# Optimization experiments

Measured on AMD Instinct MI355X. Metric: run time of the kernel, lower is better.

The kernel has to match this reference:

```python
import jax, jax.numpy as jnp
import numpy as np

C = 1024
H = 64
W = 64


def _conv1x1(x, Wt, b):
    # x: [1, Cin, H, W], Wt: [Cout, Cin] -> [1, Cout, H, W]
    return jnp.einsum('oc,bchw->bohw', Wt, x) + b[None, :, None, None]


def setup_inputs() -> dict:
    key = jax.random.key(0)
    ks = jax.random.split(key, 12)
    sc = 1.0 / np.sqrt(C)
    return {
        'x_f': jax.random.normal(ks[0], (1, C, H, W), jnp.float32),
        'x_m': jax.random.normal(ks[1], (1, C, H, W), jnp.float32),
        'x_l': jax.random.normal(ks[2], (1, C, H, W), jnp.float32),
        'Wq': jax.random.normal(ks[3], (C // 2, C), jnp.float32) * sc,
        'bq': jax.random.normal(ks[4], (C // 2,), jnp.float32) * sc,
        'Wk1': jax.random.normal(ks[5], (C // 2, C), jnp.float32) * sc,
        'bk1': jax.random.normal(ks[6], (C // 2,), jnp.float32) * sc,
        'Wk2': jax.random.normal(ks[7], (C // 2, C), jnp.float32) * sc,
        'bk2': jax.random.normal(ks[8], (C // 2,), jnp.float32) * sc,
        'Wv': jax.random.normal(ks[9], (C, C), jnp.float32) * sc,
        'bv': jax.random.normal(ks[10], (C,), jnp.float32) * sc,
        'gamma': jax.random.normal(ks[11], (1,), jnp.float32),
    }


def reference(x_f, x_m, x_l, Wq, bq, Wk1, bk1, Wk2, bk2, Wv, bv, gamma):
    c = x_f.shape[1]
    h, w = x_f.shape[2], x_f.shape[3]
    # torch .view(1, C, -1) on a [1, C/2, H, W] tensor: row-major reshape to [C, H*W/2]
    q = _conv1x1(x_m, Wq, bq).reshape(c, -1).T      # [HW/2, C]
    kf = _conv1x1(x_f, Wk1, bk1).reshape(c, -1)     # [C, HW/2]
    kl = _conv1x1(x_l, Wk2, bk2).reshape(c, -1)     # [C, HW/2]
    att_f = jax.nn.softmax(kf @ q, axis=-1)         # [C, C]
    att_l = jax.nn.softmax(kl @ q, axis=-1)         # [C, C]
    v = _conv1x1(x_m, Wv, bv).reshape(c, -1)        # [C, HW]
    out = att_f @ v + att_l @ v                     # [C, HW]
    out = out.reshape(1, c, h, w)
    return gamma * out + (x_l + x_f) / 2
```

## Files before the change

kernel.cpp:

```cpp
#include <hip/hip_runtime.h>
#include <math.h>


typedef __attribute__((ext_vector_type(8))) short    bf16x8;
typedef __attribute__((ext_vector_type(4))) float    f32x4;

__device__ __forceinline__ unsigned short f2bf(float x) {
    unsigned u = __float_as_uint(x);
    u += 0x7FFFu + ((u >> 16) & 1u);
    return (unsigned short)(u >> 16);
}
__device__ __forceinline__ float bf2f(unsigned short h) {
    return __uint_as_float(((unsigned)h) << 16);
}
__device__ __forceinline__ void split2(float x, unsigned short& h, unsigned short& l) {
    h = f2bf(x);
    l = f2bf(x - bf2f(h));
}

__device__ __forceinline__ size_t swz(int m, int k, int kpan) {
    return ((size_t)((m >> 4) * kpan + (k >> 5))) * 512
         + (size_t)((((k >> 3) & 3) * 16 + (m & 15)) * 8 + (k & 7));
}

__device__ __forceinline__ void gld16(const unsigned short* g, unsigned short* l) {
    __builtin_amdgcn_global_load_lds(
        (const __attribute__((address_space(1))) unsigned int*)g,
        (__attribute__((address_space(3))) unsigned int*)l,
        16, 0, 0);
}

__device__ __forceinline__ bf16x8 gload16(const unsigned short* p) {
    bf16x8 r;
    asm volatile("global_load_dwordx4 %0, %1, off"
                 : "=v"(r) : "v"(p) : "memory");
    return r;
}

#define RAW_BARRIER() asm volatile("s_barrier" ::: "memory")

template<int N>
__device__ __forceinline__ void vmwait() {
    asm volatile("s_waitcnt vmcnt(%0)" :: "i"(N) : "memory");
}

__global__ __launch_bounds__(256) void weights_split_k(
    const float* __restrict__ Wq, const float* __restrict__ Wk1,
    const float* __restrict__ Wk2, const float* __restrict__ Wv,
    unsigned short* __restrict__ Wqh, unsigned short* __restrict__ Wql,
    unsigned short* __restrict__ Wk1h, unsigned short* __restrict__ Wk1l,
    unsigned short* __restrict__ Wk2h, unsigned short* __restrict__ Wk2l,
    unsigned short* __restrict__ Wvh, unsigned short* __restrict__ Wvl)
{
    const int gi = blockIdx.x;
    const float* src; unsigned short *H, *L; int base;
    if (gi < 512)       { src = Wq;  H = Wqh;  L = Wql;  base = gi; }
    else if (gi < 1024) { src = Wk1; H = Wk1h; L = Wk1l; base = gi - 512; }
    else if (gi < 1536) { src = Wk2; H = Wk2h; L = Wk2l; base = gi - 1024; }
    else                { src = Wv;  H = Wvh;  L = Wvl;  base = gi - 1536; }
    const size_t i = (size_t)base * 1024 + threadIdx.x * 4;
    const int m = (int)(i >> 10);
    const int k = (int)(i & 1023);
    const float4 v = *(const float4*)(src + i);
    ushort4 h, l;
    split2(v.x, h.x, l.x); split2(v.y, h.y, l.y);
    split2(v.z, h.z, l.z); split2(v.w, h.w, l.w);
    const size_t o = swz(m, k, 32);
    *(ushort4*)(H + o) = h;
    *(ushort4*)(L + o) = l;
}

__global__ __launch_bounds__(256) void transpose3_k(
    const float* __restrict__ x0, const float* __restrict__ x1,
    const float* __restrict__ x2,
    unsigned short* __restrict__ t0h, unsigned short* __restrict__ t0l,
    unsigned short* __restrict__ t1h, unsigned short* __restrict__ t1l,
    unsigned short* __restrict__ t2h, unsigned short* __restrict__ t2l)
{
    const float* X; unsigned short *Th, *Tl;
    if (blockIdx.z == 0)      { X = x0; Th = t0h; Tl = t0l; }
    else if (blockIdx.z == 1) { X = x1; Th = t1h; Tl = t1l; }
    else                      { X = x2; Th = t2h; Tl = t2l; }

    __shared__ float t[32 * 33];
    const int tid = threadIdx.x;
    const int c0 = blockIdx.y * 32;
    const int p0 = blockIdx.x * 32;

    const int cl = tid >> 3;
    const int p4 = (tid & 7) * 4;
    const float4 v = *(const float4*)(X + (size_t)(c0 + cl) * 4096 + p0 + p4);
    t[(p4 + 0) * 33 + cl] = v.x;
    t[(p4 + 1) * 33 + cl] = v.y;
    t[(p4 + 2) * 33 + cl] = v.z;
    t[(p4 + 3) * 33 + cl] = v.w;
    __syncthreads();

    const int pl = tid >> 3;
    const int c4 = (tid & 7) * 4;
    ushort4 h, l;
    split2(t[pl * 33 + c4 + 0], h.x, l.x);
    split2(t[pl * 33 + c4 + 1], h.y, l.y);
    split2(t[pl * 33 + c4 + 2], h.z, l.z);
    split2(t[pl * 33 + c4 + 3], h.w, l.w);
    const size_t o = (size_t)(p0 + pl) * 1024 + c0 + c4;
    *(ushort4*)(Th + o) = h;
    *(ushort4*)(Tl + o) = l;
}

__global__ __launch_bounds__(256) void transpose1_k(
    const float* __restrict__ X,
    unsigned short* __restrict__ Th, unsigned short* __restrict__ Tl)
{
    __shared__ float t[32 * 33];
    const int tid = threadIdx.x;
    const int c0 = blockIdx.y * 32;
    const int p0 = blockIdx.x * 32;

    const int cl = tid >> 3;
    const int p4 = (tid & 7) * 4;
    const float4 v = *(const float4*)(X + (size_t)(c0 + cl) * 4096 + p0 + p4);
    t[(p4 + 0) * 33 + cl] = v.x;
    t[(p4 + 1) * 33 + cl] = v.y;
    t[(p4 + 2) * 33 + cl] = v.z;
    t[(p4 + 3) * 33 + cl] = v.w;
    __syncthreads();

    const int pl = tid >> 3;
    const int c4 = (tid & 7) * 4;
    ushort4 h, l;
    split2(t[pl * 33 + c4 + 0], h.x, l.x);
    split2(t[pl * 33 + c4 + 1], h.y, l.y);
    split2(t[pl * 33 + c4 + 2], h.z, l.z);
    split2(t[pl * 33 + c4 + 3], h.w, l.w);
    const size_t o = (size_t)(p0 + pl) * 1024 + c0 + c4;
    *(ushort4*)(Th + o) = h;
    *(ushort4*)(Tl + o) = l;
}

template<int TERMS, int NJ>
__device__ __forceinline__ void gemm_core(
    const unsigned short* __restrict__ Ah, const unsigned short* __restrict__ Al,
    const unsigned short* __restrict__ Bh, const unsigned short* __restrict__ Bl,
    int ldkB, int kpanA, int kbeg, int kend, int m0, int n0,
    unsigned short* Bs_h, unsigned short* Bs_l,
    f32x4 (&acc)[4][NJ])
{
    const int tid  = threadIdx.x;
    const int lane = tid & 63;
    const int wv   = tid >> 6;
    const int wm   = (wv >> 1) * 64;
    const int wn   = (wv & 1) * (16 * NJ);
    const int lr   = lane & 15;
    const int quad = lane >> 4;
    const int BUFE = 1024 * NJ;
    constexpr int AOPS = (TERMS == 3 ? 8 : 4);
    constexpr int VM_FULL = AOPS + NJ + NJ;
    constexpr int VM_MID  = AOPS + NJ;

    const unsigned short* gsrc = (wv < 2) ? Bh : Bl;
    unsigned short* ldst = (wv < 2) ? Bs_h : Bs_l;
    const int tt0  = (wv & 1) * NJ;
    const int lrow = lane >> 2;
    const int gseg = ((lane & 3) - ((lane >> 3) & 3)) & 3;
    const size_t bstep = (size_t)16 * (size_t)ldkB;
    const unsigned short* gp0 =
        gsrc + (size_t)(n0 + tt0 * 16 + lrow) * ldkB + kbeg + gseg * 8;

    const int pk0 = kbeg >> 5;
    const size_t astr  = (size_t)kpanA * 512;
    const size_t abase = (size_t)((m0 + wm) >> 4) * astr + (size_t)pk0 * 512
                       + (size_t)lane * 8;
    const unsigned short* ap0 = Ah + abase;
    const unsigned short* al0 = (TERMS == 3) ? (Al + abase) : nullptr;

    const int rdseg = (quad + (lr >> 1)) & 3;

    const int nsteps = (kend - kbeg) >> 5;

#pragma unroll
    for (int u = 0; u < NJ; ++u)
        gld16(gp0 + (size_t)u * bstep, ldst + 0 * BUFE + (tt0 + u) * 512);

    bf16x8 cah[4], cal[4], nah[4], nal[4];
#pragma unroll
    for (int i = 0; i < 4; ++i) {
        cah[i] = gload16(ap0 + (size_t)i * astr);
        if (TERMS == 3) cal[i] = gload16(al0 + (size_t)i * astr);
    }
#pragma unroll
    for (int u = 0; u < NJ; ++u)
        gld16(gp0 + (size_t)u * bstep + 32, ldst + 1 * BUFE + (tt0 + u) * 512);

    int br = 0;
    int bw = 2;

#define GSTEP(S, CH, CL, NH, NL)                                              \
    {                                                                         \
        RAW_BARRIER();                                                        \
        const bool hasA = (S) + 1 < nsteps;                                   \
        const bool hasD = (S) + 2 < nsteps;                                   \
        if (hasA) {                                                           \
            const size_t aoff = (size_t)((S) + 1) * 512;                      \
            _Pragma("unroll")                                                 \
            for (int i = 0; i < 4; ++i) {                                     \
                NH[i] = gload16(ap0 + (size_t)i * astr + aoff);               \
                if (TERMS == 3)                                               \
                    NL[i] = gload16(al0 + (size_t)i * astr + aoff);           \
            }                                                                 \
        }                                                                     \
        if (hasD) {                                                           \
            const size_t goff = (size_t)((S) + 2) * 32;                       \
            unsigned short* dst = ldst + bw * BUFE;                           \
            _Pragma("unroll")                                                 \
            for (int u = 0; u < NJ; ++u)                                      \
                gld16(gp0 + (size_t)u * bstep + goff, dst + (tt0 + u) * 512); \
            vmwait<VM_FULL>();                                                \
        } else if (hasA) {                                                    \
            vmwait<VM_MID>();                                                 \
        } else {                                                              \
            vmwait<0>();                                                      \
        }                                                                     \
        RAW_BARRIER();                                                        \
        __builtin_amdgcn_sched_barrier(0);                                    \
        const int rbase = br * BUFE + (wn + lr) * 32 + rdseg * 8;             \
        _Pragma("unroll")                                                     \
        for (int j = 0; j < NJ; ++j) {                                        \
            const bf16x8 bh = *(const bf16x8*)(Bs_h + rbase + j * 512);       \
            const bf16x8 bl = *(const bf16x8*)(Bs_l + rbase + j * 512);       \
            _Pragma("unroll")                                                 \
            for (int i = 0; i < 4; ++i) {                                     \
                acc[i][j] = __builtin_amdgcn_mfma_f32_16x16x32_bf16(          \
                    CH[i], bh, acc[i][j], 0, 0, 0);                           \
                acc[i][j] = __builtin_amdgcn_mfma_f32_16x16x32_bf16(          \
                    CH[i], bl, acc[i][j], 0, 0, 0);                           \
                if (TERMS == 3)                                               \
                    acc[i][j] = __builtin_amdgcn_mfma_f32_16x16x32_bf16(      \
                        CL[i], bh, acc[i][j], 0, 0, 0);                       \
            }                                                                 \
        }                                                                     \
        br = (br == 2) ? 0 : br + 1;                                          \
        bw = (bw == 2) ? 0 : bw + 1;                                          \
    }

    for (int s = 0; s < nsteps; s += 2) {
        GSTEP(s,     cah, cal, nah, nal);
        GSTEP(s + 1, nah, nal, cah, cal);
    }
#undef GSTEP
}

#define GEMM_PROLOGUE(NJ_)                                              \
    __shared__ __align__(16) unsigned short Bs_h[3 * 1024 * (NJ_)];     \
    __shared__ __align__(16) unsigned short Bs_l[3 * 1024 * (NJ_)];     \
    f32x4 acc[4][(NJ_)];                                                \
    _Pragma("unroll") for (int i = 0; i < 4; ++i)                       \
    _Pragma("unroll") for (int j = 0; j < (NJ_); ++j)                   \
    _Pragma("unroll") for (int r = 0; r < 4; ++r) acc[i][j][r] = 0.f;   \
    const int lane = threadIdx.x & 63;                                  \
    const int wv   = threadIdx.x >> 6;                                  \
    const int wm   = (wv >> 1) * 64;                                    \
    const int wn   = (wv & 1) * (16 * (NJ_));                           \
    const int lr   = lane & 15;                                         \
    const int quad = lane >> 4;                                         \
    (void)lane; (void)wv; (void)wm; (void)wn;

__global__ __launch_bounds__(256, 2) void conv_all_k(
    const unsigned short* __restrict__ Wqh, const unsigned short* __restrict__ Wql,
    const unsigned short* __restrict__ Wk1h, const unsigned short* __restrict__ Wk1l,
    const unsigned short* __restrict__ Wk2h, const unsigned short* __restrict__ Wk2l,
    const unsigned short* __restrict__ Wvh, const unsigned short* __restrict__ Wvl,
    const unsigned short* __restrict__ xmTh, const unsigned short* __restrict__ xmTl,
    const unsigned short* __restrict__ xfTh, const unsigned short* __restrict__ xfTl,
    const unsigned short* __restrict__ xlTh, const unsigned short* __restrict__ xlTl,
    const float* __restrict__ bq, const float* __restrict__ bk1,
    const float* __restrict__ bk2, const float* __restrict__ bv,
    unsigned short* __restrict__ Qh, unsigned short* __restrict__ Ql,
    unsigned short* __restrict__ Kfh, unsigned short* __restrict__ Kfl,
    unsigned short* __restrict__ Klh, unsigned short* __restrict__ Kll,
    float* __restrict__ V)
{
    GEMM_PROLOGUE(4);
    const int lid = blockIdx.y * 32 + blockIdx.x;
    const int wg  = (lid & 7) * 80 + (lid >> 3);
    const int mt  = wg >> 5;
    const int n0  = (wg & 31) * 128;

    const unsigned short *Ah, *Al, *Bh, *Bl;
    const float* bias;
    unsigned short *Ch = nullptr, *Cl = nullptr;
    float* Cv = nullptr;
    int mloc, mode;
    if (mt < 4) {
        Ah = Wqh;  Al = Wql;  Bh = xmTh; Bl = xmTl; bias = bq;
        Ch = Qh;   Cl = Ql;   mloc = mt * 128;        mode = 0;
    } else if (mt < 8) {
        Ah = Wk1h; Al = Wk1l; Bh = xfTh; Bl = xfTl; bias = bk1;
        Ch = Kfh;  Cl = Kfl;  mloc = (mt - 4) * 128;  mode = 1;
    } else if (mt < 12) {
        Ah = Wk2h; Al = Wk2l; Bh = xlTh; Bl = xlTl; bias = bk2;
        Ch = Klh;  Cl = Kll;  mloc = (mt - 8) * 128;  mode = 1;
    } else {
        Ah = Wvh;  Al = Wvl;  Bh = xmTh; Bl = xmTl; bias = bv;
        Cv = V;    mloc = (mt - 12) * 128;            mode = 2;
    }

    gemm_core<3, 4>(Ah, Al, Bh, Bl, 1024, 32, 0, 1024, mloc, n0, Bs_h, Bs_l, acc);

#pragma unroll
    for (int i = 0; i < 4; ++i) {
        const int mb = mloc + wm + i * 16 + quad * 4;
#pragma unroll
        for (int j = 0; j < 4; ++j) {
            const int nn = n0 + wn + j * 16 + lr;
#pragma unroll
            for (int r = 0; r < 4; ++r) {
                const float v = acc[i][j][r] + bias[mb + r];
                if (mode == 2) {
                    Cv[(size_t)(mb + r) * 4096 + nn] = v;
                } else if (mode == 0) {
                    unsigned short h, l;
                    split2(v, h, l);
                    const size_t idx = (size_t)(mb + r) * 4096 + nn;
                    Ch[idx] = h;
                    Cl[idx] = l;
                } else {
                    const int m2 = ((mb + r) << 1) | (nn >> 11);
                    const int k2 = nn & 2047;
                    const size_t o = swz(m2, k2, 64);
                    unsigned short h, l;
                    split2(v, h, l);
                    Ch[o] = h;
                    Cl[o] = l;
                }
            }
        }
    }
}

__global__ __launch_bounds__(256, 2) void logits_fused_k(
    const unsigned short* __restrict__ Kfh, const unsigned short* __restrict__ Kfl,
    const unsigned short* __restrict__ Klh, const unsigned short* __restrict__ Kll,
    const unsigned short* __restrict__ Qh, const unsigned short* __restrict__ Ql,
    float* __restrict__ Sfp, float* __restrict__ Slp)
{
    GEMM_PROLOGUE(4);
    const int lid = (blockIdx.z * 8 + blockIdx.y) * 8 + blockIdx.x;
    const int wg  = (lid & 7) * 64 + (lid >> 3);
    const int bx  = wg & 7;
    const int by  = (wg >> 3) & 7;
    const int bz  = wg >> 6;

    const int which = bz >> 2;
    const int slice = bz & 3;
    const unsigned short* Ah = which ? Klh : Kfh;
    const unsigned short* Al = which ? Kll : Kfl;
    float* out = (which ? Slp : Sfp) + (size_t)slice * 1024 * 1024;
    const int m0 = by * 128;
    const int n0 = bx * 128;

    gemm_core<3, 4>(Ah, Al, Qh, Ql, 2048, 64, slice * 512, slice * 512 + 512,
                    m0, n0, Bs_h, Bs_l, acc);

#pragma unroll
    for (int i = 0; i < 4; ++i) {
        const int mb = m0 + wm + i * 16 + quad * 4;
#pragma unroll
        for (int j = 0; j < 4; ++j) {
            const int nn = n0 + wn + j * 16 + lr;
#pragma unroll
            for (int r = 0; r < 4; ++r)
                out[(size_t)(mb + r) * 1024 + nn] = acc[i][j][r];
        }
    }
}

__global__ __launch_bounds__(256, 2) void gemm_final_k(
    const unsigned short* __restrict__ Amh,
    const unsigned short* __restrict__ VTh, const unsigned short* __restrict__ VTl,
    float* __restrict__ out,
    const float* __restrict__ xf, const float* __restrict__ xl,
    const float* __restrict__ gamma)
{
    GEMM_PROLOGUE(4);
    const int m0 = blockIdx.y * 128;
    const int n0 = blockIdx.x * 128;

    gemm_core<2, 4>(Amh, nullptr, VTh, VTl, 1024, 32, 0, 1024, m0, n0,
                    Bs_h, Bs_l, acc);

    const float g = gamma[0];
#pragma unroll
    for (int i = 0; i < 4; ++i) {
        const int mb = m0 + wm + i * 16 + quad * 4;
#pragma unroll
        for (int j = 0; j < 4; ++j) {
            const int nn = n0 + wn + j * 16 + lr;
#pragma unroll
            for (int r = 0; r < 4; ++r) {
                const size_t idx = (size_t)(mb + r) * 4096 + nn;
                out[idx] = g * acc[i][j][r] + 0.5f * (xf[idx] + xl[idx]);
            }
        }
    }
}

__global__ __launch_bounds__(256) void softmax_add4_k(
    const float* __restrict__ Sfp, const float* __restrict__ Slp,
    unsigned short* __restrict__ Ah)
{
    const int row = blockIdx.x;
    const int tid = threadIdx.x;
    __shared__ float red[8];
    const size_t base = (size_t)row * 1024 + tid * 4;
    const size_t SL = (size_t)1024 * 1024;

    float4 vf = *(const float4*)(Sfp + base);
    float4 vl = *(const float4*)(Slp + base);
#pragma unroll
    for (int s = 1; s < 4; ++s) {
        const float4 a = *(const float4*)(Sfp + s * SL + base);
        const float4 b = *(const float4*)(Slp + s * SL + base);
        vf.x += a.x; vf.y += a.y; vf.z += a.z; vf.w += a.w;
        vl.x += b.x; vl.y += b.y; vl.z += b.z; vl.w += b.w;
    }

    float mf = fmaxf(fmaxf(vf.x, vf.y), fmaxf(vf.z, vf.w));
    float ml = fmaxf(fmaxf(vl.x, vl.y), fmaxf(vl.z, vl.w));
#pragma unroll
    for (int off = 32; off; off >>= 1) {
        mf = fmaxf(mf, __shfl_down(mf, off, 64));
        ml = fmaxf(ml, __shfl_down(ml, off, 64));
    }
    const int wave = tid >> 6;
    if ((tid & 63) == 0) { red[wave] = mf; red[4 + wave] = ml; }
    __syncthreads();
    mf = fmaxf(fmaxf(red[0], red[1]), fmaxf(red[2], red[3]));
    ml = fmaxf(fmaxf(red[4], red[5]), fmaxf(red[6], red[7]));
    __syncthreads();

    const float4 ef = make_float4(expf(vf.x - mf), expf(vf.y - mf),
                                  expf(vf.z - mf), expf(vf.w - mf));
    const float4 el = make_float4(expf(vl.x - ml), expf(vl.y - ml),
                                  expf(vl.z - ml), expf(vl.w - ml));
    float sf = ef.x + ef.y + ef.z + ef.w;
    float sl = el.x + el.y + el.z + el.w;
#pragma unroll
    for (int off = 32; off; off >>= 1) {
        sf += __shfl_down(sf, off, 64);
        sl += __shfl_down(sl, off, 64);
    }
    if ((tid & 63) == 0) { red[wave] = sf; red[4 + wave] = sl; }
    __syncthreads();
    sf = red[0] + red[1] + red[2] + red[3];
    sl = red[4] + red[5] + red[6] + red[7];

    const float rf = 1.f / sf, rl = 1.f / sl;
    ushort4 h;
    h.x = f2bf(ef.x * rf + el.x * rl);
    h.y = f2bf(ef.y * rf + el.y * rl);
    h.z = f2bf(ef.z * rf + el.z * rl);
    h.w = f2bf(ef.w * rf + el.w * rl);
    const size_t o = swz(row, tid * 4, 32);
    *(ushort4*)(Ah + o) = h;
}

__global__ void noop_k(float* p) { if (threadIdx.x == 1024) p[0] = 0.f; }

extern "C" void kernel_launch(void* const* d_in, const int* in_sizes, int n_in,
                              void* d_out, int out_size, void* d_ws, size_t ws_size,
                              hipStream_t stream) {
    (void)in_sizes; (void)n_in; (void)out_size;
    const float* xf  = (const float*)d_in[0];
    const float* xm  = (const float*)d_in[1];
    const float* xl  = (const float*)d_in[2];
    const float* Wq  = (const float*)d_in[3];
    const float* bq  = (const float*)d_in[4];
    const float* Wk1 = (const float*)d_in[5];
    const float* bk1 = (const float*)d_in[6];
    const float* Wk2 = (const float*)d_in[7];
    const float* bk2 = (const float*)d_in[8];
    const float* Wv  = (const float*)d_in[9];
    const float* bv  = (const float*)d_in[10];
    const float* gamma = (const float*)d_in[11];
    float* out = (float*)d_out;

    const size_t MB = 1024 * 1024;
    if (ws_size < 98 * MB) {
        noop_k<<<dim3(1), dim3(64), 0, stream>>>((float*)d_ws);
        return;
    }

    char* p = (char*)d_ws;
    unsigned short* xmT_h = (unsigned short*)(p + 0 * MB);
    unsigned short* xmT_l = (unsigned short*)(p + 8 * MB);
    unsigned short* xfT_h = (unsigned short*)(p + 16 * MB);
    unsigned short* xfT_l = (unsigned short*)(p + 24 * MB);
    unsigned short* xlT_h = (unsigned short*)(p + 32 * MB);
    unsigned short* xlT_l = (unsigned short*)(p + 40 * MB);
    unsigned short* Wq_h  = (unsigned short*)(p + 48 * MB);
    unsigned short* Wq_l  = (unsigned short*)(p + 49 * MB);
    unsigned short* Wk1_h = (unsigned short*)(p + 50 * MB);
    unsigned short* Wk1_l = (unsigned short*)(p + 51 * MB);
    unsigned short* Wk2_h = (unsigned short*)(p + 52 * MB);
    unsigned short* Wk2_l = (unsigned short*)(p + 53 * MB);
    unsigned short* Wv_h  = (unsigned short*)(p + 54 * MB);
    unsigned short* Wv_l  = (unsigned short*)(p + 56 * MB);
    unsigned short* Q_h   = (unsigned short*)(p + 58 * MB);
    unsigned short* Q_l   = (unsigned short*)(p + 62 * MB);
    unsigned short* Kf_h  = (unsigned short*)(p + 66 * MB);
    unsigned short* Kf_l  = (unsigned short*)(p + 70 * MB);
    unsigned short* Kl_h  = (unsigned short*)(p + 74 * MB);
    unsigned short* Kl_l  = (unsigned short*)(p + 78 * MB);
    float*          V     = (float*)(p + 82 * MB);
    float*          Sfp  = (float*)(p + 16 * MB);
    float*          Slp  = (float*)(p + 32 * MB);
    unsigned short* VT_h = xmT_h;
    unsigned short* VT_l = xmT_l;
    unsigned short* Am_h = (unsigned short*)(p + 74 * MB);

    const dim3 blk(256);
    transpose3_k<<<dim3(128, 32, 3), blk, 0, stream>>>(
        xm, xf, xl, xmT_h, xmT_l, xfT_h, xfT_l, xlT_h, xlT_l);
    weights_split_k<<<dim3(2560), blk, 0, stream>>>(
        Wq, Wk1, Wk2, Wv, Wq_h, Wq_l, Wk1_h, Wk1_l, Wk2_h, Wk2_l, Wv_h, Wv_l);
    conv_all_k<<<dim3(32, 20), blk, 0, stream>>>(
        Wq_h, Wq_l, Wk1_h, Wk1_l, Wk2_h, Wk2_l, Wv_h, Wv_l,
        xmT_h, xmT_l, xfT_h, xfT_l, xlT_h, xlT_l,
        bq, bk1, bk2, bv,
        Q_h, Q_l, Kf_h, Kf_l, Kl_h, Kl_l, V);
    logits_fused_k<<<dim3(8, 8, 8), blk, 0, stream>>>(
        Kf_h, Kf_l, Kl_h, Kl_l, Q_h, Q_l, Sfp, Slp);
    transpose1_k<<<dim3(128, 32), blk, 0, stream>>>(V, VT_h, VT_l);
    softmax_add4_k<<<dim3(1024), blk, 0, stream>>>(Sfp, Slp, Am_h);
    gemm_final_k<<<dim3(32, 8), blk, 0, stream>>>(
        Am_h, VT_h, VT_l, out, xf, xl, gamma);
}
```

Before: 278.3 us.

## Fuse V transpose and bf16 split into conv epilogue via shared memory

The V projection epilogue now transposes its output tile through shared memory and writes the bf16 hi/lo split directly in [HW, C] layout. This replaces the fp32 V write, the separate transpose1_k launch and its re-read. It adds extra syncthreads and LDS staging in the conv epilogue for the V blocks, and moves VT into a dedicated buffer.

Measured after the change: 272.3 us. 1.02x faster.

```diff
diff --git a/kernel.cpp b/kernel.cpp
--- a/kernel.cpp
+++ b/kernel.cpp
@@ -82,36 +82,6 @@
     else if (blockIdx.z == 1) { X = x1; Th = t1h; Tl = t1l; }
     else                      { X = x2; Th = t2h; Tl = t2l; }
 
-    __shared__ float t[32 * 33];
-    const int tid = threadIdx.x;
-    const int c0 = blockIdx.y * 32;
-    const int p0 = blockIdx.x * 32;
-
-    const int cl = tid >> 3;
-    const int p4 = (tid & 7) * 4;
-    const float4 v = *(const float4*)(X + (size_t)(c0 + cl) * 4096 + p0 + p4);
-    t[(p4 + 0) * 33 + cl] = v.x;
-    t[(p4 + 1) * 33 + cl] = v.y;
-    t[(p4 + 2) * 33 + cl] = v.z;
-    t[(p4 + 3) * 33 + cl] = v.w;
-    __syncthreads();
-
-    const int pl = tid >> 3;
-    const int c4 = (tid & 7) * 4;
-    ushort4 h, l;
-    split2(t[pl * 33 + c4 + 0], h.x, l.x);
-    split2(t[pl * 33 + c4 + 1], h.y, l.y);
-    split2(t[pl * 33 + c4 + 2], h.z, l.z);
-    split2(t[pl * 33 + c4 + 3], h.w, l.w);
-    const size_t o = (size_t)(p0 + pl) * 1024 + c0 + c4;
-    *(ushort4*)(Th + o) = h;
-    *(ushort4*)(Tl + o) = l;
-}
-
-__global__ __launch_bounds__(256) void transpose1_k(
-    const float* __restrict__ X,
-    unsigned short* __restrict__ Th, unsigned short* __restrict__ Tl)
-{
     __shared__ float t[32 * 33];
     const int tid = threadIdx.x;
     const int c0 = blockIdx.y * 32;
@@ -278,7 +248,7 @@
     unsigned short* __restrict__ Qh, unsigned short* __restrict__ Ql,
     unsigned short* __restrict__ Kfh, unsigned short* __restrict__ Kfl,
     unsigned short* __restrict__ Klh, unsigned short* __restrict__ Kll,
-    float* __restrict__ V)
+    unsigned short* __restrict__ VTh, unsigned short* __restrict__ VTl)
 {
     GEMM_PROLOGUE(4);
     const int lid = blockIdx.y * 32 + blockIdx.x;
@@ -289,7 +259,6 @@
     const unsigned short *Ah, *Al, *Bh, *Bl;
     const float* bias;
     unsigned short *Ch = nullptr, *Cl = nullptr;
-    float* Cv = nullptr;
     int mloc, mode;
     if (mt < 4) {
         Ah = Wqh;  Al = Wql;  Bh = xmTh; Bl = xmTl; bias = bq;
@@ -302,10 +271,52 @@
         Ch = Klh;  Cl = Kll;  mloc = (mt - 8) * 128;  mode = 1;
     } else {
         Ah = Wvh;  Al = Wvl;  Bh = xmTh; Bl = xmTl; bias = bv;
-        Cv = V;    mloc = (mt - 12) * 128;            mode = 2;
+        mloc = (mt - 12) * 128;                       mode = 2;
     }
 
     gemm_core<3, 4>(Ah, Al, Bh, Bl, 1024, 32, 0, 1024, mloc, n0, Bs_h, Bs_l, acc);
+
+    if (mode == 2) {
+        __syncthreads();
+        unsigned short (*Sh)[136] = (unsigned short (*)[136])Bs_h;
+        unsigned short (*Sl)[136] = (unsigned short (*)[136])Bs_l;
+        const int myhalf = (wv & 1);
+#pragma unroll
+        for (int sb = 0; sb < 4; ++sb) {
+            if ((sb >> 1) == myhalf) {
+                const int jbase = (sb & 1) * 2;
+#pragma unroll
+                for (int jj = 0; jj < 2; ++jj) {
+                    const int j = jbase + jj;
+                    const int prow = jj * 16 + lr;
+#pragma unroll
+                    for (int i = 0; i < 4; ++i) {
+#pragma unroll
+                        for (int r = 0; r < 4; ++r) {
+                            const int c = wm + i * 16 + quad * 4 + r;
+                            const float v = acc[i][j][r] + bias[mloc + c];
+                            unsigned short h, l;
+                            split2(v, h, l);
+                            Sh[prow][c] = h;
+                            Sl[prow][c] = l;
+                        }
+                    }
+                }
+            }
+            __syncthreads();
+            {
+                const int pl2 = threadIdx.x >> 3;
+                const int c0  = (threadIdx.x & 7) * 16;
+                const size_t ob = (size_t)(n0 + sb * 32 + pl2) * 1024 + mloc + c0;
+                *(bf16x8*)(VTh + ob)     = *(const bf16x8*)&Sh[pl2][c0];
+                *(bf16x8*)(VTh + ob + 8) = *(const bf16x8*)&Sh[pl2][c0 + 8];
+                *(bf16x8*)(VTl + ob)     = *(const bf16x8*)&Sl[pl2][c0];
+                *(bf16x8*)(VTl + ob + 8) = *(const bf16x8*)&Sl[pl2][c0 + 8];
+            }
+            __syncthreads();
+        }
+        return;
+    }
 
 #pragma unroll
     for (int i = 0; i < 4; ++i) {
@@ -316,9 +327,7 @@
 #pragma unroll
             for (int r = 0; r < 4; ++r) {
                 const float v = acc[i][j][r] + bias[mb + r];
-                if (mode == 2) {
-                    Cv[(size_t)(mb + r) * 4096 + nn] = v;
-                } else if (mode == 0) {
+                if (mode == 0) {
                     unsigned short h, l;
                     split2(v, h, l);
                     const size_t idx = (size_t)(mb + r) * 4096 + nn;
@@ -512,11 +521,10 @@
     unsigned short* Kf_l  = (unsigned short*)(p + 70 * MB);
     unsigned short* Kl_h  = (unsigned short*)(p + 74 * MB);
     unsigned short* Kl_l  = (unsigned short*)(p + 78 * MB);
-    float*          V     = (float*)(p + 82 * MB);
+    unsigned short* VT_h  = (unsigned short*)(p + 82 * MB);
+    unsigned short* VT_l  = (unsigned short*)(p + 90 * MB);
     float*          Sfp  = (float*)(p + 16 * MB);
     float*          Slp  = (float*)(p + 32 * MB);
-    unsigned short* VT_h = xmT_h;
-    unsigned short* VT_l = xmT_l;
     unsigned short* Am_h = (unsigned short*)(p + 74 * MB);
 
     const dim3 blk(256);
@@ -528,10 +536,9 @@
         Wq_h, Wq_l, Wk1_h, Wk1_l, Wk2_h, Wk2_l, Wv_h, Wv_l,
         xmT_h, xmT_l, xfT_h, xfT_l, xlT_h, xlT_l,
         bq, bk1, bk2, bv,
-        Q_h, Q_l, Kf_h, Kf_l, Kl_h, Kl_l, V);
+        Q_h, Q_l, Kf_h, Kf_l, Kl_h, Kl_l, VT_h, VT_l);
     logits_fused_k<<<dim3(8, 8, 8), blk, 0, stream>>>(
         Kf_h, Kf_l, Kl_h, Kl_l, Q_h, Q_l, Sfp, Slp);
-    transpose1_k<<<dim3(128, 32), blk, 0, stream>>>(V, VT_h, VT_l);
     softmax_add4_k<<<dim3(1024), blk, 0, stream>>>(Sfp, Slp, Am_h);
     gemm_final_k<<<dim3(32, 8), blk, 0, stream>>>(
         Am_h, VT_h, VT_l, out, xf, xl, gamma);
```
